# Performance work log

Measured on AMD Instinct MI355X. Metric: run time of the kernel, lower is better.

The kernel has to match this reference:

```python
import jax, jax.numpy as jnp
import numpy as np

DIM = 512
HEADS = 8
HEAD_DIM = 64
INNER = HEADS * HEAD_DIM  # 512
FF = DIM * 2
EPS = 1e-5


def layernorm(x, g, b):
    mu = jnp.mean(x, axis=-1, keepdims=True)
    var = jnp.var(x, axis=-1, keepdims=True)
    return (x - mu) * jax.lax.rsqrt(var + EPS) * g + b


def setup_inputs() -> dict:
    key = jax.random.key(0)
    ks = jax.random.split(key, 10)
    s = lambda fan_in: 1.0 / np.sqrt(fan_in)
    return {
        "x": jax.random.normal(ks[0], (4, 2048, DIM), dtype=jnp.float32),
        "ln1_g": jnp.ones((DIM,), jnp.float32),
        "ln1_b": jnp.zeros((DIM,), jnp.float32),
        "w_qkv": jax.random.normal(ks[1], (DIM, 3 * INNER), jnp.float32) * s(DIM),
        "w_out": jax.random.normal(ks[2], (INNER, DIM), jnp.float32) * s(INNER),
        "b_out": jnp.zeros((DIM,), jnp.float32),
        "ln2_g": jnp.ones((DIM,), jnp.float32),
        "ln2_b": jnp.zeros((DIM,), jnp.float32),
        "w1": jax.random.normal(ks[3], (DIM, FF), jnp.float32) * s(DIM),
        "b1": jnp.zeros((FF,), jnp.float32),
        "w2": jax.random.normal(ks[4], (FF, DIM), jnp.float32) * s(FF),
        "b2": jnp.zeros((DIM,), jnp.float32),
    }


def reference(x, ln1_g, ln1_b, w_qkv, w_out, b_out, ln2_g, ln2_b, w1, b1, w2, b2):
    b, n, _ = x.shape
    # --- pre-LN MHSA ---
    h = layernorm(x, ln1_g, ln1_b)
    qkv = h @ w_qkv  # [b, n, 3*inner]
    q, k, v = jnp.split(qkv, 3, axis=-1)
    to_heads = lambda t: t.reshape(b, n, HEADS, HEAD_DIM).transpose(0, 2, 1, 3)
    q, k, v = to_heads(q), to_heads(k), to_heads(v)
    scores = jnp.einsum('bhid,bhjd->bhij', q, k) * (HEAD_DIM ** -0.5)
    attn = jax.nn.softmax(scores, axis=-1)
    attended = jnp.einsum('bhij,bhjd->bhid', attn, v)
    attended = attended.transpose(0, 2, 1, 3).reshape(b, n, INNER)
    x = attended @ w_out + b_out + x
    # --- pre-LN MLP ---
    h = layernorm(x, ln2_g, ln2_b)
    h = jax.nn.gelu(h @ w1 + b1, approximate=False)
    x = h @ w2 + b2 + x
    return x
```

## Files before the change

### kernel.cpp

```cpp
#include <hip/hip_runtime.h>
#include <math.h>


#define TOKENS 8192
#define SEQ    2048
typedef unsigned short u16;
typedef __attribute__((ext_vector_type(8))) _Float16 h8;
typedef __attribute__((ext_vector_type(4))) float f32x4;
typedef __attribute__((ext_vector_type(4))) unsigned short u16x4;

__device__ __forceinline__ u16 f2h(float f) {
    _Float16 h = (_Float16)f;
    return __builtin_bit_cast(u16, h);
}
__device__ __forceinline__ unsigned int pk2h(float a, float b) {
    return __builtin_bit_cast(unsigned int, __builtin_amdgcn_cvt_pkrtz(a, b));
}
__device__ __forceinline__ void a16(void* lds, const void* g) {
    __builtin_amdgcn_global_load_lds(
        (const __attribute__((address_space(1))) unsigned int*)g,
        (__attribute__((address_space(3))) unsigned int*)lds, 16, 0, 0);
}
__device__ __forceinline__ float gelu_exact(float v) {
    return 0.5f * v * (1.0f + erff(v * 0.70710678118654752f));
}

__global__ __launch_bounds__(256) void prep_k(const float* __restrict__ wqkv,
                                              const float* __restrict__ wout,
                                              const float* __restrict__ w1,
                                              const float* __restrict__ w2,
                                              u16* __restrict__ dqkv,
                                              u16* __restrict__ dout,
                                              u16* __restrict__ d1,
                                              u16* __restrict__ d2,
                                              const float* __restrict__ x,
                                              const float* __restrict__ g,
                                              const float* __restrict__ bta,
                                              u16* __restrict__ oh) {
    const int tid = threadIdx.x;
    if (blockIdx.x >= 512) {
        const int lane = tid & 63;
        const int row  = ((blockIdx.x - 512) << 2) + (tid >> 6);
        const float* xr = x + ((size_t)row << 9) + (lane << 3);
        float v[8];
        *(float4*)&v[0] = *(const float4*)xr;
        *(float4*)&v[4] = *(const float4*)(xr + 4);
        float s = 0.f, ss = 0.f;
#pragma unroll
        for (int i = 0; i < 8; i++) { s += v[i]; ss += v[i] * v[i]; }
#pragma unroll
        for (int m = 32; m; m >>= 1) {
            s  += __shfl_xor(s, m, 64);
            ss += __shfl_xor(ss, m, 64);
        }
        const float mu   = s * (1.0f / 512.0f);
        const float rstd = rsqrtf(ss * (1.0f / 512.0f) - mu * mu + 1e-5f);
        float gg[8], bb[8];
        *(float4*)&gg[0] = *(const float4*)(g + (lane << 3));
        *(float4*)&gg[4] = *(const float4*)(g + (lane << 3) + 4);
        *(float4*)&bb[0] = *(const float4*)(bta + (lane << 3));
        *(float4*)&bb[4] = *(const float4*)(bta + (lane << 3) + 4);
        union { u16 us[8]; uint4 q; } H;
#pragma unroll
        for (int i = 0; i < 8; i++) H.us[i] = f2h((v[i] - mu) * rstd * gg[i] + bb[i]);
        *(uint4*)&oh[((size_t)row << 9) + (lane << 3)] = H.q;
        return;
    }
    __shared__ float t[64][65];
    int b = blockIdx.x;
    const float* src; u16* dst; int K, N, n0, k0;
    if (b < 192)      { src = wqkv; dst = dqkv; K = 512;  N = 1536; n0 = (b % 24) << 6; k0 = (b / 24) << 6; }
    else if (b < 256) { b -= 192; src = wout; dst = dout; K = 512;  N = 512;  n0 = (b & 7) << 6;  k0 = (b >> 3) << 6; }
    else if (b < 384) { b -= 256; src = w1;   dst = d1;   K = 512;  N = 1024; n0 = (b & 15) << 6; k0 = (b >> 4) << 6; }
    else              { b -= 384; src = w2;   dst = d2;   K = 1024; N = 512;  n0 = (b & 7) << 6;  k0 = (b >> 3) << 6; }
    {
        const int kr = tid >> 2, nc = (tid & 3) << 4;
        const float* p = src + (size_t)(k0 + kr) * N + n0 + nc;
#pragma unroll
        for (int i = 0; i < 4; i++)
            *(float4*)&t[kr][nc + (i << 2)] = *(const float4*)(p + (i << 2));
    }
    __syncthreads();
    {
        const int nr = tid >> 2, kc = (tid & 3) << 4;
        union { u16 us[16]; uint4 q[2]; } H;
#pragma unroll
        for (int i = 0; i < 16; i++) H.us[i] = f2h(t[kc + i][nr]);
        const size_t o = (size_t)(n0 + nr) * K + k0 + kc;
        *(uint4*)&dst[o] = H.q[0];
        *(uint4*)&dst[o + 8] = H.q[1];
    }
}

__global__ __launch_bounds__(256) void ln_k(const float* __restrict__ x,
                                            const float* __restrict__ g,
                                            const float* __restrict__ bta,
                                            u16* __restrict__ oh) {
    const int lane = threadIdx.x & 63;
    const int row  = (blockIdx.x << 2) + (threadIdx.x >> 6);
    const float* xr = x + ((size_t)row << 9) + (lane << 3);
    float v[8];
    *(float4*)&v[0] = *(const float4*)xr;
    *(float4*)&v[4] = *(const float4*)(xr + 4);
    float s = 0.f, ss = 0.f;
#pragma unroll
    for (int i = 0; i < 8; i++) { s += v[i]; ss += v[i] * v[i]; }
#pragma unroll
    for (int m = 32; m; m >>= 1) {
        s  += __shfl_xor(s, m, 64);
        ss += __shfl_xor(ss, m, 64);
    }
    const float mu   = s * (1.0f / 512.0f);
    const float rstd = rsqrtf(ss * (1.0f / 512.0f) - mu * mu + 1e-5f);
    float gg[8], bb[8];
    *(float4*)&gg[0] = *(const float4*)(g + (lane << 3));
    *(float4*)&gg[4] = *(const float4*)(g + (lane << 3) + 4);
    *(float4*)&bb[0] = *(const float4*)(bta + (lane << 3));
    *(float4*)&bb[4] = *(const float4*)(bta + (lane << 3) + 4);
    union { u16 us[8]; uint4 q; } H;
#pragma unroll
    for (int i = 0; i < 8; i++) H.us[i] = f2h((v[i] - mu) * rstd * gg[i] + bb[i]);
    *(uint4*)&oh[((size_t)row << 9) + (lane << 3)] = H.q;
}

template <int EPI>
__global__ __launch_bounds__(256, 3) void sgemm_k(
    const u16* __restrict__ A, const u16* __restrict__ B,
    const float* __restrict__ bias, const float* __restrict__ res,
    float* __restrict__ Cf, u16* __restrict__ Ch, u16* __restrict__ Dh,
    int M, int N, int K) {
    __shared__ u16 sm[24576];
    const int tid = threadIdx.x;
    const int lane = tid & 63, wv = tid >> 6;
    const int col = lane & 15, quad = lane >> 4;
    const int wm = (wv & 1) << 6, wn = (wv >> 1) << 6;
    const int bm = blockIdx.y << 7, bn = blockIdx.x << 7;

    const int r0 = tid >> 2,         c0 = (tid & 3) ^ ((r0 >> 1) & 3);
    const int r1 = (tid + 256) >> 2, c1 = (tid & 3) ^ ((r1 >> 1) & 3);
    const u16* Ag0 = A + (size_t)(bm + r0) * K + c0 * 8;
    const u16* Ag1 = A + (size_t)(bm + r1) * K + c1 * 8;
    const u16* Bg0 = B + (size_t)(bn + r0) * K + c0 * 8;
    const u16* Bg1 = B + (size_t)(bn + r1) * K + c1 * 8;
    const int lw0 = wv * 512, lw1 = wv * 512 + 2048;
    const int swz = (col >> 1) & 3;
    const f32x4 z4 = {0.f, 0.f, 0.f, 0.f};
    f32x4 acc[4][4] = {{z4,z4,z4,z4},{z4,z4,z4,z4},{z4,z4,z4,z4},{z4,z4,z4,z4}};

    a16(&sm[lw0],        Ag0);       a16(&sm[lw1],        Ag1);
    a16(&sm[lw0 + 4096], Bg0);       a16(&sm[lw1 + 4096], Bg1);
    a16(&sm[8192 + lw0],        Ag0 + 32);  a16(&sm[8192 + lw1],        Ag1 + 32);
    a16(&sm[8192 + lw0 + 4096], Bg0 + 32);  a16(&sm[8192 + lw1 + 4096], Bg1 + 32);

    int cb = 0;
    int nb = 16384;
    for (int k0 = 0; k0 < K; k0 += 32) {
        if (k0 + 32 < K) {
            asm volatile("s_waitcnt vmcnt(4) lgkmcnt(0)\n\ts_barrier" ::: "memory");
        } else {
            asm volatile("s_waitcnt vmcnt(0) lgkmcnt(0)\n\ts_barrier" ::: "memory");
        }
        if (k0 + 64 < K) {
            const int kn = k0 + 64;
            a16(&sm[nb + lw0],        Ag0 + kn);  a16(&sm[nb + lw1],        Ag1 + kn);
            a16(&sm[nb + lw0 + 4096], Bg0 + kn);  a16(&sm[nb + lw1 + 4096], Bg1 + kn);
        }
        h8 af[4];
#pragma unroll
        for (int mt = 0; mt < 4; mt++) {
            const int ra = cb + (wm + (mt << 4) + col) * 32 + ((quad ^ swz) << 3);
            af[mt] = *(const h8*)&sm[ra];
        }
#pragma unroll
        for (int nt = 0; nt < 4; nt++) {
            const int rb = cb + 4096 + (wn + (nt << 4) + col) * 32 + ((quad ^ swz) << 3);
            h8 bf = *(const h8*)&sm[rb];
#pragma unroll
            for (int mt = 0; mt < 4; mt++)
                acc[mt][nt] = __builtin_amdgcn_mfma_f32_16x16x32_f16(af[mt], bf, acc[mt][nt], 0, 0, 0);
        }
        nb = cb;
        cb = (cb == 16384) ? 0 : cb + 8192;
    }

    if constexpr (EPI == 0) {
        if (bn >= 1024) {
            const int hd0  = (bn - 1024) >> 6;
            const int b8   = (bm >> 11) << 3;
            const int keyb = bm & 2047;
            __syncthreads();
#pragma unroll
            for (int hf = 0; hf < 2; hf++) {
                if ((wv >> 1) == hf) {
#pragma unroll
                    for (int mt = 0; mt < 4; mt++)
#pragma unroll
                    for (int rr = 0; rr < 4; rr++) {
                        const int key = wm + (mt << 4) + (quad << 2) + rr;
#pragma unroll
                        for (int nt = 0; nt < 4; nt++) {
                            const int dl = (nt << 4) + col;
                            sm[dl * 136 + key] = f2h(acc[mt][nt][rr]);
                        }
                    }
                }
                __syncthreads();
                {
                    const int d = tid >> 2;
#pragma unroll
                    for (int c = 0; c < 4; c++) {
                        const int key0 = ((((tid & 3) << 2) + c) << 3);
                        const size_t gb = ((size_t)(b8 + hd0 + hf) << 17)
                                        + ((size_t)d << 11) + keyb + key0;
                        *(uint4*)&Dh[gb] = *(const uint4*)&sm[d * 136 + key0];
                    }
                }
                __syncthreads();
            }
            return;
        }
    }

    float bs[4];
    if constexpr (EPI >= 1) {
#pragma unroll
        for (int nt = 0; nt < 4; nt++) bs[nt] = bias[bn + wn + (nt << 4) + col];
    }
#pragma unroll
    for (int mt = 0; mt < 4; mt++) {
#pragma unroll
        for (int rr = 0; rr < 4; rr++) {
            const int row = bm + wm + (mt << 4) + (quad << 2) + rr;
#pragma unroll
            for (int nt = 0; nt < 4; nt++) {
                const int colg = bn + wn + (nt << 4) + col;
                float v = acc[mt][nt][rr];
                if constexpr (EPI == 0) {
                    const int b = row >> 11, key = row & 2047;
                    if (bn < 512) {
                        Cf[((size_t)row << 9) + colg] = v;
                    } else {
                        const int hd = (colg - 512) >> 6, d = colg & 63;
                        Ch[((size_t)((b << 3) + hd) << 17) + (key << 6) + d] = f2h(v);
                    }
                } else if constexpr (EPI == 2) {
                    Ch[(size_t)row * N + colg] = f2h(gelu_exact(v + bs[nt]));
                } else {
                    const size_t o = (size_t)row * N + colg;
                    Cf[o] = v + bs[nt] + res[o];
                }
            }
        }
    }
}

__global__ __launch_bounds__(256, 4) void attn_k(const float* __restrict__ q,
                                                 const u16* __restrict__ kh,
                                                 const u16* __restrict__ vth,
                                                 u16* __restrict__ ah) {
    __shared__ u16 sm[20480];
    const int tid = threadIdx.x;
    const int lane = tid & 63, wv = tid >> 6;
    const int col = lane & 15, quad = lane >> 4;
    const int qt = blockIdx.x, bh = blockIdx.y;
    const int b = bh >> 3, h = bh & 7;
    const size_t tok0 = (size_t)b * SEQ;
    const size_t bhK = (size_t)bh << 17;
    const int q0 = qt << 6;

    h8 qf[2];
    {
        const int qrow = q0 + (wv << 4) + col;
        const float* qp = q + ((tok0 + qrow) << 9) + (h << 6) + (quad << 3);
#pragma unroll
        for (int kc = 0; kc < 2; kc++) {
            float v[8];
            *(float4*)&v[0] = *(const float4*)(qp + (kc << 5));
            *(float4*)&v[4] = *(const float4*)(qp + (kc << 5) + 4);
            union { u16 us[8]; h8 v8; } H;
#pragma unroll
            for (int i = 0; i < 8; i++) H.us[i] = f2h(v[i] * 0.125f);
            qf[kc] = H.v8;
        }
    }

    const f32x4 z4 = {0.f, 0.f, 0.f, 0.f};
    f32x4 o[4] = {z4, z4, z4, z4};
    float m_run = -1e30f, l_run = 0.f;

    size_t kbz[2], vbz[2];
    int doff[2];
#pragma unroll
    for (int j = 0; j < 2; j++) {
        const int C = (((j << 2) + wv) << 6) + lane;
        const int sr = C >> 3, sp = (C & 7) ^ (sr & 7);
        kbz[j] = bhK + ((size_t)sr << 6) + (sp << 3);
        vbz[j] = bhK + ((size_t)sr << 11) + (sp << 3);
        doff[j] = (((j << 2) + wv) << 9);
    }

#pragma unroll
    for (int j = 0; j < 2; j++) a16(&sm[doff[j]], kh + kbz[j]);
#pragma unroll
    for (int j = 0; j < 2; j++) a16(&sm[8192 + doff[j]], vth + vbz[j]);
#pragma unroll
    for (int j = 0; j < 2; j++) a16(&sm[4096 + doff[j]], kh + kbz[j] + 4096);

    int ib = 0;
    const int prow = (wv << 4) + col;
    const int p64 = prow << 6, p7 = prow & 7;
    for (int jt = 0; jt < 32; jt++, ib ^= 1) {
        if (jt < 31) {
            asm volatile("s_waitcnt vmcnt(2) lgkmcnt(0)\n\ts_barrier" ::: "memory");
        } else {
            asm volatile("s_waitcnt vmcnt(0) lgkmcnt(0)\n\ts_barrier" ::: "memory");
        }
        if (jt < 31) {
            const size_t vo = (size_t)(jt + 1) << 6;
            const int vb = 8192 + ((ib ^ 1) << 12);
#pragma unroll
            for (int j = 0; j < 2; j++) a16(&sm[vb + doff[j]], vth + vbz[j] + vo);
        }

        const int cb = ib << 12;
        f32x4 st[4] = {z4, z4, z4, z4};
        __builtin_amdgcn_s_setprio(1);
#pragma unroll
        for (int kb = 0; kb < 4; kb++) {
            const int key = (kb << 4) + col;
            const int r64 = key << 6, k7 = key & 7;
#pragma unroll
            for (int kc = 0; kc < 2; kc++) {
                const int ofs = cb + r64 + ((((kc << 2) + quad) ^ k7) << 3);
                h8 kf = *(const h8*)&sm[ofs];
                st[kb] = __builtin_amdgcn_mfma_f32_16x16x32_f16(kf, qf[kc], st[kb], 0, 0, 0);
            }
        }
        __builtin_amdgcn_s_setprio(0);

        float mx = st[0][0];
#pragma unroll
        for (int kb = 0; kb < 4; kb++)
#pragma unroll
            for (int r = 0; r < 4; r++) mx = fmaxf(mx, st[kb][r]);
        mx = fmaxf(mx, __shfl_xor(mx, 16));
        mx = fmaxf(mx, __shfl_xor(mx, 32));
        if (__any(mx > m_run + 7.5f)) {
            const float mn  = fmaxf(m_run, mx);
            const float alp = __expf(m_run - mn);
            m_run = mn;
            l_run *= alp;
            float aO[4];
#pragma unroll
            for (int r = 0; r < 4; r++) aO[r] = __shfl(alp, (quad << 2) + r);
#pragma unroll
            for (int db = 0; db < 4; db++) {
                o[db][0] *= aO[0]; o[db][1] *= aO[1];
                o[db][2] *= aO[2]; o[db][3] *= aO[3];
            }
        }
        float p[16];
        float rs = 0.0f;
#pragma unroll
        for (int kb = 0; kb < 4; kb++)
#pragma unroll
            for (int r = 0; r < 4; r++) {
                float e = __expf(st[kb][r] - m_run);
                p[(kb << 2) + r] = e;
                rs += e;
            }
        rs += __shfl_xor(rs, 16);
        rs += __shfl_xor(rs, 32);
        l_run += rs;
#pragma unroll
        for (int kb = 0; kb < 4; kb++) {
            uint2 w;
            w.x = pk2h(p[(kb << 2) + 0], p[(kb << 2) + 1]);
            w.y = pk2h(p[(kb << 2) + 2], p[(kb << 2) + 3]);
            const int c = (kb << 1) + (quad >> 1);
            *(uint2*)&sm[16384 + p64 + ((c ^ p7) << 3) + ((quad & 1) << 2)] = w;
        }

        asm volatile("s_waitcnt lgkmcnt(0)\n\ts_barrier" ::: "memory");

        if (jt < 30) {
            const size_t ko = (size_t)(jt + 2) << 12;
            const int kb2 = ib << 12;
#pragma unroll
            for (int j = 0; j < 2; j++) a16(&sm[kb2 + doff[j]], kh + kbz[j] + ko);
        }

        h8 pf[2];
#pragma unroll
        for (int kc = 0; kc < 2; kc++)
            pf[kc] = *(const h8*)&sm[16384 + p64 + ((((kc << 2) + quad) ^ p7) << 3)];

        const int vbase = 8192 + (ib << 12);
        __builtin_amdgcn_s_setprio(1);
#pragma unroll
        for (int db = 0; db < 4; db++) {
            const int d = (db << 4) + col;
            const int v64 = vbase + (d << 6), d7 = d & 7;
#pragma unroll
            for (int kc = 0; kc < 2; kc++) {
                h8 vf = *(const h8*)&sm[v64 + ((((kc << 2) + quad) ^ d7) << 3)];
                o[db] = __builtin_amdgcn_mfma_f32_16x16x32_f16(pf[kc], vf, o[db], 0, 0, 0);
            }
        }
        __builtin_amdgcn_s_setprio(0);
    }

    float linv[4];
#pragma unroll
    for (int r = 0; r < 4; r++) linv[r] = 1.0f / __shfl(l_run, (quad << 2) + r);
#pragma unroll
    for (int r = 0; r < 4; r++) {
        const size_t rowo = ((tok0 + q0 + (wv << 4) + (quad << 2) + r) << 9)
                            + (h << 6) + col;
#pragma unroll
        for (int db = 0; db < 4; db++)
            ah[rowo + (db << 4)] = f2h(o[db][r] * linv[r]);
    }
}

extern "C" void kernel_launch(void* const* d_in, const int* in_sizes, int n_in,
                              void* d_out, int out_size, void* d_ws, size_t ws_size,
                              hipStream_t stream) {
    const float* x     = (const float*)d_in[0];
    const float* ln1_g = (const float*)d_in[1];
    const float* ln1_b = (const float*)d_in[2];
    const float* w_qkv = (const float*)d_in[3];
    const float* w_out = (const float*)d_in[4];
    const float* b_out = (const float*)d_in[5];
    const float* ln2_g = (const float*)d_in[6];
    const float* ln2_b = (const float*)d_in[7];
    const float* w1    = (const float*)d_in[8];
    const float* b1    = (const float*)d_in[9];
    const float* w2    = (const float*)d_in[10];
    const float* b2    = (const float*)d_in[11];
    float* out = (float*)d_out;

    u16* wqkvh = (u16*)d_ws;
    u16* wouth = wqkvh + 1536 * 512;
    u16* w1h   = wouth + 512 * 512;
    u16* w2h   = w1h + 1024 * 512;
    u16* hbuf  = w2h + 512 * 1024;
    float* qbuf = (float*)(hbuf + (size_t)TOKENS * 512);
    float* x2   = qbuf;
    u16* kh  = (u16*)(qbuf + (size_t)TOKENS * 512);
    u16* vth = kh + (size_t)32 * 131072;
    u16* gh  = kh;

    prep_k<<<2560, 256, 0, stream>>>(w_qkv, w_out, w1, w2, wqkvh, wouth, w1h, w2h,
                                     x, ln1_g, ln1_b, hbuf);
    sgemm_k<0><<<dim3(12, 64), 256, 0, stream>>>(hbuf, wqkvh, nullptr, nullptr,
                                                 qbuf, kh, vth, TOKENS, 1536, 512);
    attn_k<<<dim3(32, 32), 256, 0, stream>>>(qbuf, kh, vth, hbuf);
    sgemm_k<1><<<dim3(4, 64), 256, 0, stream>>>(hbuf, wouth, b_out, x,
                                                x2, nullptr, nullptr, TOKENS, 512, 512);
    ln_k<<<TOKENS / 4, 256, 0, stream>>>(x2, ln2_g, ln2_b, hbuf);
    sgemm_k<2><<<dim3(8, 64), 256, 0, stream>>>(hbuf, w1h, b1, nullptr,
                                                nullptr, gh, nullptr, TOKENS, 1024, 512);
    sgemm_k<3><<<dim3(4, 64), 256, 0, stream>>>(gh, w2h, b2, x2,
                                                out, nullptr, nullptr, TOKENS, 512, 1024);
}
```

Measured before the change: 238.2 us.

## Store Q as scaled fp16, triple-buffer K in attention, remap block IDs for XCDs

The QKV GEMM epilogue now writes Q as fp16 with the 1/8 softmax scale folded in, so attention no longer loads and converts fp32 Q. The attention kernel moves to a three-slot K ring buffer, issues the K prefetch at the top of each iteration, and drops one barrier per tile. This costs more LDS and lowers the occupancy hint from 4 to 3. The GEMM, attention and layernorm kernels also remap block indices so consecutive tiles land on the same XCD, aiming for better L2 locality.

```diff
diff --git a/kernel.cpp b/kernel.cpp
--- a/kernel.cpp
+++ b/kernel.cpp
@@ -39,8 +39,10 @@
                                               u16* __restrict__ oh) {
     const int tid = threadIdx.x;
     if (blockIdx.x >= 512) {
+        const int f = blockIdx.x - 512;
+        const int grp = ((f & 7) << 8) | (f >> 3);
         const int lane = tid & 63;
-        const int row  = ((blockIdx.x - 512) << 2) + (tid >> 6);
+        const int row  = (grp << 2) + (tid >> 6);
         const float* xr = x + ((size_t)row << 9) + (lane << 3);
         float v[8];
         *(float4*)&v[0] = *(const float4*)xr;
@@ -96,8 +98,10 @@
                                             const float* __restrict__ g,
                                             const float* __restrict__ bta,
                                             u16* __restrict__ oh) {
+    const int B = blockIdx.x;
+    const int grp = ((B & 7) << 8) | (B >> 3);
     const int lane = threadIdx.x & 63;
-    const int row  = (blockIdx.x << 2) + (threadIdx.x >> 6);
+    const int row  = (grp << 2) + (threadIdx.x >> 6);
     const float* xr = x + ((size_t)row << 9) + (lane << 3);
     float v[8];
     *(float4*)&v[0] = *(const float4*)xr;
@@ -134,7 +138,12 @@
     const int lane = tid & 63, wv = tid >> 6;
     const int col = lane & 15, quad = lane >> 4;
     const int wm = (wv & 1) << 6, wn = (wv >> 1) << 6;
-    const int bm = blockIdx.y << 7, bn = blockIdx.x << 7;
+
+    const int nbx  = gridDim.x;
+    const int flat = blockIdx.x + blockIdx.y * nbx;
+    const int nwg  = nbx * gridDim.y;
+    const int lid  = ((flat & 7) * (nwg >> 3)) + (flat >> 3);
+    const int bm = (lid / nbx) << 7, bn = (lid % nbx) << 7;
 
     const int r0 = tid >> 2,         c0 = (tid & 3) ^ ((r0 >> 1) & 3);
     const int r1 = (tid + 256) >> 2, c1 = (tid & 3) ^ ((r1 >> 1) & 3);
@@ -238,7 +247,7 @@
                 if constexpr (EPI == 0) {
                     const int b = row >> 11, key = row & 2047;
                     if (bn < 512) {
-                        Cf[((size_t)row << 9) + colg] = v;
+                        ((u16*)Cf)[((size_t)row << 9) + colg] = f2h(v * 0.125f);
                     } else {
                         const int hd = (colg - 512) >> 6, d = colg & 63;
                         Ch[((size_t)((b << 3) + hd) << 17) + (key << 6) + d] = f2h(v);
@@ -254,15 +263,17 @@
     }
 }
 
-__global__ __launch_bounds__(256, 4) void attn_k(const float* __restrict__ q,
+__global__ __launch_bounds__(256, 3) void attn_k(const u16* __restrict__ q,
                                                  const u16* __restrict__ kh,
                                                  const u16* __restrict__ vth,
                                                  u16* __restrict__ ah) {
-    __shared__ u16 sm[20480];
+    __shared__ u16 sm[24576];
     const int tid = threadIdx.x;
     const int lane = tid & 63, wv = tid >> 6;
     const int col = lane & 15, quad = lane >> 4;
-    const int qt = blockIdx.x, bh = blockIdx.y;
+    const int flat = blockIdx.x + (blockIdx.y << 5);
+    const int lid  = ((flat & 7) << 7) + (flat >> 3);
+    const int qt = lid & 31, bh = lid >> 5;
     const int b = bh >> 3, h = bh & 7;
     const size_t tok0 = (size_t)b * SEQ;
     const size_t bhK = (size_t)bh << 17;
@@ -271,17 +282,10 @@
     h8 qf[2];
     {
         const int qrow = q0 + (wv << 4) + col;
-        const float* qp = q + ((tok0 + qrow) << 9) + (h << 6) + (quad << 3);
-#pragma unroll
-        for (int kc = 0; kc < 2; kc++) {
-            float v[8];
-            *(float4*)&v[0] = *(const float4*)(qp + (kc << 5));
-            *(float4*)&v[4] = *(const float4*)(qp + (kc << 5) + 4);
-            union { u16 us[8]; h8 v8; } H;
-#pragma unroll
-            for (int i = 0; i < 8; i++) H.us[i] = f2h(v[i] * 0.125f);
-            qf[kc] = H.v8;
-        }
+        const u16* qp = q + ((tok0 + qrow) << 9) + (h << 6) + (quad << 3);
+#pragma unroll
+        for (int kc = 0; kc < 2; kc++)
+            qf[kc] = *(const h8*)(qp + (kc << 5));
     }
 
     const f32x4 z4 = {0.f, 0.f, 0.f, 0.f};
@@ -302,14 +306,14 @@
 #pragma unroll
     for (int j = 0; j < 2; j++) a16(&sm[doff[j]], kh + kbz[j]);
 #pragma unroll
-    for (int j = 0; j < 2; j++) a16(&sm[8192 + doff[j]], vth + vbz[j]);
+    for (int j = 0; j < 2; j++) a16(&sm[12288 + doff[j]], vth + vbz[j]);
 #pragma unroll
     for (int j = 0; j < 2; j++) a16(&sm[4096 + doff[j]], kh + kbz[j] + 4096);
 
-    int ib = 0;
     const int prow = (wv << 4) + col;
     const int p64 = prow << 6, p7 = prow & 7;
-    for (int jt = 0; jt < 32; jt++, ib ^= 1) {
+    int kcur = 0;
+    for (int jt = 0; jt < 32; jt++) {
         if (jt < 31) {
             asm volatile("s_waitcnt vmcnt(2) lgkmcnt(0)\n\ts_barrier" ::: "memory");
         } else {
@@ -317,12 +321,17 @@
         }
         if (jt < 31) {
             const size_t vo = (size_t)(jt + 1) << 6;
-            const int vb = 8192 + ((ib ^ 1) << 12);
+            const int vb = 12288 + (((jt + 1) & 1) << 12);
 #pragma unroll
             for (int j = 0; j < 2; j++) a16(&sm[vb + doff[j]], vth + vbz[j] + vo);
         }
-
-        const int cb = ib << 12;
+        if (jt < 30) {
+            const size_t ko = (size_t)(jt + 2) << 12;
+            int kt = kcur + 8192; if (kt >= 12288) kt -= 12288;
+#pragma unroll
+            for (int j = 0; j < 2; j++) a16(&sm[kt + doff[j]], kh + kbz[j] + ko);
+        }
+
         f32x4 st[4] = {z4, z4, z4, z4};
         __builtin_amdgcn_s_setprio(1);
 #pragma unroll
@@ -331,7 +340,7 @@
             const int r64 = key << 6, k7 = key & 7;
 #pragma unroll
             for (int kc = 0; kc < 2; kc++) {
-                const int ofs = cb + r64 + ((((kc << 2) + quad) ^ k7) << 3);
+                const int ofs = kcur + r64 + ((((kc << 2) + quad) ^ k7) << 3);
                 h8 kf = *(const h8*)&sm[ofs];
                 st[kb] = __builtin_amdgcn_mfma_f32_16x16x32_f16(kf, qf[kc], st[kb], 0, 0, 0);
             }
@@ -378,24 +387,17 @@
             w.x = pk2h(p[(kb << 2) + 0], p[(kb << 2) + 1]);
             w.y = pk2h(p[(kb << 2) + 2], p[(kb << 2) + 3]);
             const int c = (kb << 1) + (quad >> 1);
-            *(uint2*)&sm[16384 + p64 + ((c ^ p7) << 3) + ((quad & 1) << 2)] = w;
-        }
-
-        asm volatile("s_waitcnt lgkmcnt(0)\n\ts_barrier" ::: "memory");
-
-        if (jt < 30) {
-            const size_t ko = (size_t)(jt + 2) << 12;
-            const int kb2 = ib << 12;
-#pragma unroll
-            for (int j = 0; j < 2; j++) a16(&sm[kb2 + doff[j]], kh + kbz[j] + ko);
-        }
+            *(uint2*)&sm[20480 + p64 + ((c ^ p7) << 3) + ((quad & 1) << 2)] = w;
+        }
+
+        asm volatile("s_waitcnt lgkmcnt(0)" ::: "memory");
 
         h8 pf[2];
 #pragma unroll
         for (int kc = 0; kc < 2; kc++)
-            pf[kc] = *(const h8*)&sm[16384 + p64 + ((((kc << 2) + quad) ^ p7) << 3)];
-
-        const int vbase = 8192 + (ib << 12);
+            pf[kc] = *(const h8*)&sm[20480 + p64 + ((((kc << 2) + quad) ^ p7) << 3)];
+
+        const int vbase = 12288 + ((jt & 1) << 12);
         __builtin_amdgcn_s_setprio(1);
 #pragma unroll
         for (int db = 0; db < 4; db++) {
@@ -408,6 +410,8 @@
             }
         }
         __builtin_amdgcn_s_setprio(0);
+
+        kcur = (kcur == 8192) ? 0 : kcur + 4096;
     }
 
     float linv[4];
@@ -446,6 +450,7 @@
     u16* w2h   = w1h + 1024 * 512;
     u16* hbuf  = w2h + 512 * 1024;
     float* qbuf = (float*)(hbuf + (size_t)TOKENS * 512);
+    u16* qh16   = (u16*)qbuf;
     float* x2   = qbuf;
     u16* kh  = (u16*)(qbuf + (size_t)TOKENS * 512);
     u16* vth = kh + (size_t)32 * 131072;
@@ -454,8 +459,8 @@
     prep_k<<<2560, 256, 0, stream>>>(w_qkv, w_out, w1, w2, wqkvh, wouth, w1h, w2h,
                                      x, ln1_g, ln1_b, hbuf);
     sgemm_k<0><<<dim3(12, 64), 256, 0, stream>>>(hbuf, wqkvh, nullptr, nullptr,
-                                                 qbuf, kh, vth, TOKENS, 1536, 512);
-    attn_k<<<dim3(32, 32), 256, 0, stream>>>(qbuf, kh, vth, hbuf);
+                                                 (float*)qh16, kh, vth, TOKENS, 1536, 512);
+    attn_k<<<dim3(32, 32), 256, 0, stream>>>(qh16, kh, vth, hbuf);
     sgemm_k<1><<<dim3(4, 64), 256, 0, stream>>>(hbuf, wouth, b_out, x,
                                                 x2, nullptr, nullptr, TOKENS, 512, 512);
     ln_k<<<TOKENS / 4, 256, 0, stream>>>(x2, ln2_g, ln2_b, hbuf);
```

After: 244.9 us. 2.8% more time.
